# Kernel tuning notes

Hardware: AMD Instinct MI355X
Metric: run time of the kernel (lower is better)

Reference implementation:

```python
import jax, jax.numpy as jnp
import numpy as np

N_LEVELS = 8
BASE_RES = 16
LOG2_T = 14
T = 1 << LOG2_T
WIDTH, HEIGHT = 1024, 768
NUM_GAUSSIAN = 8
PRIME_Y = np.uint32(2654435761)
CORNERS = np.array([[0, 0], [1, 0], [0, 1], [1, 1]], dtype=np.uint32)


def _level_resolutions():
    bx = np.exp((np.log(WIDTH) - np.log(BASE_RES)) / (N_LEVELS - 1))
    by = np.exp((np.log(HEIGHT) - np.log(BASE_RES)) / (N_LEVELS - 1))
    return [(int(np.floor(BASE_RES * bx ** l)), int(np.floor(BASE_RES * by ** l)))
            for l in range(N_LEVELS)]


def hash_encode(x, hashidxs, table):
    # x: [N,2] in [0,1]; hashidxs: [N] int; table: [V, L, T, 2]
    feats = []
    offs = jnp.asarray(CORNERS)  # [4,2] uint32
    hv = hashidxs.astype(jnp.int32)[:, None]  # [N,1]
    for l, (rx, ry) in enumerate(_level_resolutions()):
        res = jnp.array([rx, ry], dtype=x.dtype)
        pos = x * res                      # [N,2]
        p0 = jnp.floor(pos)
        w = pos - p0                       # bilinear weights, [N,2]
        c = p0.astype(jnp.uint32)[:, None, :] + offs[None]  # [N,4,2]
        h = (c[..., 0] * jnp.uint32(1)) ^ (c[..., 1] * PRIME_Y)
        idx = (h & jnp.uint32(T - 1)).astype(jnp.int32)      # [N,4]
        f = table[hv, l, idx]              # [N,4,2] gather per corner
        wx, wy = w[:, 0:1], w[:, 1:2]
        ww = jnp.concatenate([(1 - wx) * (1 - wy), wx * (1 - wy),
                              (1 - wx) * wy, wx * wy], axis=1)  # [N,4]
        feats.append(jnp.sum(f * ww[..., None], axis=1))        # [N,2]
    return jnp.concatenate(feats, axis=-1)  # [N,16]


def gaussian_act(x, sigma=0.1):
    return jnp.exp(x * x * (-1.0 / (2.0 * sigma * sigma)))


def setup_inputs() -> dict:
    key = jax.random.key(0)
    ks = jax.random.split(key, 8)
    N = 2 ** 21
    V = 20
    x = jax.random.uniform(ks[0], (N, 2), dtype=jnp.float32)
    hashidxs = jax.random.randint(ks[1], (N,), 0, V, dtype=jnp.int32)
    color = jax.random.uniform(ks[2], (N, 3), dtype=jnp.float32)
    table = jax.random.normal(ks[3], (V, N_LEVELS, T, 2), dtype=jnp.float32) * 1e-2
    w1 = jax.random.normal(ks[4], (16, 32), dtype=jnp.float32) * (1.0 / np.sqrt(16))
    b1 = jax.random.normal(ks[5], (32,), dtype=jnp.float32) * 0.01
    w2 = jax.random.normal(ks[6], (32, 3 * NUM_GAUSSIAN), dtype=jnp.float32) * (1.0 / np.sqrt(32))
    b2 = jax.random.normal(ks[7], (3 * NUM_GAUSSIAN,), dtype=jnp.float32) * 0.01
    return {"x": x, "hashidxs": hashidxs, "color": color, "table": table,
            "w1": w1, "b1": b1, "w2": w2, "b2": b2}


def reference(x, hashidxs, color, table, w1, b1, w2, b2):
    H = hash_encode(x, hashidxs, table)            # [N,16]
    h1 = gaussian_act(H @ w1 + b1)                 # [N,32]
    raw = h1 @ w2 + b2                             # [N,24]
    G = NUM_GAUSSIAN
    weight = jnp.exp(raw[..., :G])
    mu = jax.nn.sigmoid(raw[..., G:2 * G])
    inv_sigma = jnp.exp(raw[..., 2 * G:3 * G])
    return mu, inv_sigma, weight, H
```

## Files before the change

### kernel.cpp

```cpp
#include <hip/hip_runtime.h>
#include <cmath>

#define NLEV 8
#define TSZ 16384
#define PRIME 2654435761u

struct Res { int rx[NLEV]; int ry[NLEV]; };

__global__ __launch_bounds__(256) void pg_kernel(
    const float* __restrict__ x,
    const int*   __restrict__ hashidxs,
    const float* __restrict__ table,
    const float* __restrict__ w1,
    const float* __restrict__ b1,
    const float* __restrict__ w2,
    const float* __restrict__ b2,
    float* __restrict__ out,
    int N, Res res)
{
    int i = blockIdx.x * blockDim.x + threadIdx.x;
    if (i >= N) return;

    float2 xv = ((const float2*)x)[i];
    int hv = hashidxs[i];
    const float* tb_base = table + (size_t)hv * (NLEV * TSZ * 2);

    float H[16];
    #pragma unroll
    for (int l = 0; l < NLEV; ++l) {
        float fx = (float)res.rx[l], fy = (float)res.ry[l];
        float posx = xv.x * fx, posy = xv.y * fy;
        float p0x = floorf(posx), p0y = floorf(posy);
        float wx = posx - p0x, wy = posy - p0y;
        unsigned cx = (unsigned)p0x, cy = (unsigned)p0y;
        const float* tb = tb_base + (size_t)l * (TSZ * 2);
        unsigned hy0 = cy * PRIME;
        unsigned hy1 = (cy + 1u) * PRIME;
        unsigned i00 = ( cx        ^ hy0) & (TSZ - 1);
        unsigned i10 = ((cx + 1u)  ^ hy0) & (TSZ - 1);
        unsigned i01 = ( cx        ^ hy1) & (TSZ - 1);
        unsigned i11 = ((cx + 1u)  ^ hy1) & (TSZ - 1);
        float2 f00 = *(const float2*)(tb + 2u * i00);
        float2 f10 = *(const float2*)(tb + 2u * i10);
        float2 f01 = *(const float2*)(tb + 2u * i01);
        float2 f11 = *(const float2*)(tb + 2u * i11);
        float w00 = (1.f - wx) * (1.f - wy);
        float w10 = wx * (1.f - wy);
        float w01 = (1.f - wx) * wy;
        float w11 = wx * wy;
        H[2*l]   = fmaf(f00.x, w00, fmaf(f10.x, w10, fmaf(f01.x, w01, f11.x * w11)));
        H[2*l+1] = fmaf(f00.y, w00, fmaf(f10.y, w10, fmaf(f01.y, w01, f11.y * w11)));
    }

    float h1[32];
    #pragma unroll
    for (int j = 0; j < 32; ++j) {
        float s = b1[j];
        #pragma unroll
        for (int k = 0; k < 16; ++k) s = fmaf(H[k], w1[k * 32 + j], s);
        h1[j] = __expf(-50.f * s * s);
    }

    float raw[24];
    #pragma unroll
    for (int j = 0; j < 24; ++j) {
        float s = b2[j];
        #pragma unroll
        for (int k = 0; k < 32; ++k) s = fmaf(h1[k], w2[k * 24 + j], s);
        raw[j] = s;
    }

    float wt[8], mu[8], isg[8];
    #pragma unroll
    for (int g = 0; g < 8; ++g) {
        wt[g]  = __expf(raw[g]);
        mu[g]  = 1.f / (1.f + __expf(-raw[8 + g]));
        isg[g] = __expf(raw[16 + g]);
    }

    size_t N8 = (size_t)N * 8;
    float4* o;
    o = (float4*)(out) + (size_t)i * 2;
    o[0] = make_float4(mu[0], mu[1], mu[2], mu[3]);
    o[1] = make_float4(mu[4], mu[5], mu[6], mu[7]);
    o = (float4*)(out + N8) + (size_t)i * 2;
    o[0] = make_float4(isg[0], isg[1], isg[2], isg[3]);
    o[1] = make_float4(isg[4], isg[5], isg[6], isg[7]);
    o = (float4*)(out + 2 * N8) + (size_t)i * 2;
    o[0] = make_float4(wt[0], wt[1], wt[2], wt[3]);
    o[1] = make_float4(wt[4], wt[5], wt[6], wt[7]);
    o = (float4*)(out + 3 * N8) + (size_t)i * 4;
    o[0] = make_float4(H[0],  H[1],  H[2],  H[3]);
    o[1] = make_float4(H[4],  H[5],  H[6],  H[7]);
    o[2] = make_float4(H[8],  H[9],  H[10], H[11]);
    o[3] = make_float4(H[12], H[13], H[14], H[15]);
}

extern "C" void kernel_launch(void* const* d_in, const int* in_sizes, int n_in,
                              void* d_out, int out_size, void* d_ws, size_t ws_size,
                              hipStream_t stream) {
    const float* x        = (const float*)d_in[0];
    const int*   hashidxs = (const int*)  d_in[1];
    const float* table    = (const float*)d_in[3];
    const float* w1       = (const float*)d_in[4];
    const float* b1       = (const float*)d_in[5];
    const float* w2       = (const float*)d_in[6];
    const float* b2       = (const float*)d_in[7];
    float* out = (float*)d_out;
    int N = in_sizes[0] / 2;

    Res res;
    double bx = std::exp((std::log((double)1024) - std::log((double)16)) / 7.0);
    double by = std::exp((std::log((double)768)  - std::log((double)16)) / 7.0);
    for (int l = 0; l < NLEV; ++l) {
        res.rx[l] = (int)std::floor(16.0 * std::pow(bx, (double)l));
        res.ry[l] = (int)std::floor(16.0 * std::pow(by, (double)l));
    }

    dim3 block(256), grid((unsigned)((N + 255) / 256));
    hipLaunchKernelGGL(pg_kernel, grid, block, 0, stream,
                       x, hashidxs, table, w1, b1, w2, b2, out, N, res);
}
```

Baseline: 675.8 us.

## Bucket points by hash table index and remap workgroups per XCD

Adds a counting-sort pre-pass (zero, histogram, scan, scatter) that groups points by their hash-table index. The main kernel then processes points in sorted order, so each workgroup touches mostly one 1 MB table slice. Workgroup IDs are also remapped so that consecutive sorted chunks land on the same XCD, keeping each XCD's L2 working set to a few tables. The cost is four extra launches, an extra pass over x and hashidxs, and output writes that become scattered rather than coalesced. If the workspace is too small it falls back to the original kernel.

```diff
diff --git a/kernel.cpp b/kernel.cpp
--- a/kernel.cpp
+++ b/kernel.cpp
@@ -4,25 +4,19 @@
 #define NLEV 8
 #define TSZ 16384
 #define PRIME 2654435761u
+#define NBINS 32
+
+typedef float fx2 __attribute__((ext_vector_type(2)));
 
 struct Res { int rx[NLEV]; int ry[NLEV]; };
 
-__global__ __launch_bounds__(256) void pg_kernel(
-    const float* __restrict__ x,
-    const int*   __restrict__ hashidxs,
+__device__ __forceinline__ void compute_point(
+    fx2 xv, int hv, int p,
     const float* __restrict__ table,
-    const float* __restrict__ w1,
-    const float* __restrict__ b1,
-    const float* __restrict__ w2,
-    const float* __restrict__ b2,
-    float* __restrict__ out,
-    int N, Res res)
-{
-    int i = blockIdx.x * blockDim.x + threadIdx.x;
-    if (i >= N) return;
-
-    float2 xv = ((const float2*)x)[i];
-    int hv = hashidxs[i];
+    const float* __restrict__ w1, const float* __restrict__ b1,
+    const float* __restrict__ w2, const float* __restrict__ b2,
+    float* __restrict__ out, int N, const Res& res)
+{
     const float* tb_base = table + (size_t)hv * (NLEV * TSZ * 2);
 
     float H[16];
@@ -40,10 +34,10 @@
         unsigned i10 = ((cx + 1u)  ^ hy0) & (TSZ - 1);
         unsigned i01 = ( cx        ^ hy1) & (TSZ - 1);
         unsigned i11 = ((cx + 1u)  ^ hy1) & (TSZ - 1);
-        float2 f00 = *(const float2*)(tb + 2u * i00);
-        float2 f10 = *(const float2*)(tb + 2u * i10);
-        float2 f01 = *(const float2*)(tb + 2u * i01);
-        float2 f11 = *(const float2*)(tb + 2u * i11);
+        fx2 f00 = *(const fx2*)(tb + 2u * i00);
+        fx2 f10 = *(const fx2*)(tb + 2u * i10);
+        fx2 f01 = *(const fx2*)(tb + 2u * i01);
+        fx2 f11 = *(const fx2*)(tb + 2u * i11);
         float w00 = (1.f - wx) * (1.f - wy);
         float w10 = wx * (1.f - wy);
         float w01 = (1.f - wx) * wy;
@@ -80,20 +74,102 @@
 
     size_t N8 = (size_t)N * 8;
     float4* o;
-    o = (float4*)(out) + (size_t)i * 2;
+    o = (float4*)(out) + (size_t)p * 2;
     o[0] = make_float4(mu[0], mu[1], mu[2], mu[3]);
     o[1] = make_float4(mu[4], mu[5], mu[6], mu[7]);
-    o = (float4*)(out + N8) + (size_t)i * 2;
+    o = (float4*)(out + N8) + (size_t)p * 2;
     o[0] = make_float4(isg[0], isg[1], isg[2], isg[3]);
     o[1] = make_float4(isg[4], isg[5], isg[6], isg[7]);
-    o = (float4*)(out + 2 * N8) + (size_t)i * 2;
+    o = (float4*)(out + 2 * N8) + (size_t)p * 2;
     o[0] = make_float4(wt[0], wt[1], wt[2], wt[3]);
     o[1] = make_float4(wt[4], wt[5], wt[6], wt[7]);
-    o = (float4*)(out + 3 * N8) + (size_t)i * 4;
+    o = (float4*)(out + 3 * N8) + (size_t)p * 4;
     o[0] = make_float4(H[0],  H[1],  H[2],  H[3]);
     o[1] = make_float4(H[4],  H[5],  H[6],  H[7]);
     o[2] = make_float4(H[8],  H[9],  H[10], H[11]);
     o[3] = make_float4(H[12], H[13], H[14], H[15]);
+}
+
+__global__ __launch_bounds__(256) void pg_kernel(
+    const float* __restrict__ x, const int* __restrict__ hashidxs,
+    const float* __restrict__ table,
+    const float* __restrict__ w1, const float* __restrict__ b1,
+    const float* __restrict__ w2, const float* __restrict__ b2,
+    float* __restrict__ out, int N, Res res)
+{
+    int i = blockIdx.x * blockDim.x + threadIdx.x;
+    if (i >= N) return;
+    fx2 xv = ((const fx2*)x)[i];
+    int hv = hashidxs[i];
+    compute_point(xv, hv, i, table, w1, b1, w2, b2, out, N, res);
+}
+
+__global__ void k_zero(int* __restrict__ c) {
+    int t = threadIdx.x;
+    if (t < 2 * NBINS) c[t] = 0;
+}
+
+__global__ __launch_bounds__(256) void k_hist(
+    const int* __restrict__ hashidxs, int N, int* __restrict__ hist)
+{
+    __shared__ int lh[NBINS];
+    int t = threadIdx.x;
+    if (t < NBINS) lh[t] = 0;
+    __syncthreads();
+    int i = blockIdx.x * 256 + t;
+    if (i < N) atomicAdd(&lh[hashidxs[i]], 1);
+    __syncthreads();
+    if (t < NBINS && lh[t]) atomicAdd(&hist[t], lh[t]);
+}
+
+__global__ void k_scan(const int* __restrict__ hist, int* __restrict__ cursor) {
+    if (threadIdx.x == 0 && blockIdx.x == 0) {
+        int acc = 0;
+        for (int b = 0; b < NBINS; ++b) { cursor[b] = acc; acc += hist[b]; }
+    }
+}
+
+__global__ __launch_bounds__(256) void k_scatter(
+    const float* __restrict__ x, const int* __restrict__ hashidxs, int N,
+    int* __restrict__ cursor, int* __restrict__ order, float* __restrict__ sx)
+{
+    __shared__ int lh[NBINS];
+    __shared__ int lbase[NBINS];
+    int t = threadIdx.x;
+    if (t < NBINS) lh[t] = 0;
+    __syncthreads();
+    int i = blockIdx.x * 256 + t;
+    int hv = -1, r = 0;
+    if (i < N) { hv = hashidxs[i]; r = atomicAdd(&lh[hv], 1); }
+    __syncthreads();
+    if (t < NBINS && lh[t]) lbase[t] = atomicAdd(&cursor[t], lh[t]);
+    __syncthreads();
+    if (i < N) {
+        int pos = lbase[hv] + r;
+        order[pos] = i | (hv << 24);
+        ((fx2*)sx)[pos] = ((const fx2*)x)[i];
+    }
+}
+
+__global__ __launch_bounds__(256) void pg_main(
+    const int*   __restrict__ order,
+    const float* __restrict__ sx,
+    const float* __restrict__ table,
+    const float* __restrict__ w1, const float* __restrict__ b1,
+    const float* __restrict__ w2, const float* __restrict__ b2,
+    float* __restrict__ out, int N, Res res)
+{
+    unsigned nwg  = gridDim.x, orig = blockIdx.x;
+    unsigned q = nwg / 8u, rr = nwg % 8u, xcd = orig % 8u;
+    unsigned wg = (xcd < rr ? xcd * (q + 1u) : rr * (q + 1u) + (xcd - rr) * q) + orig / 8u;
+    int j = (int)(wg * 256u + threadIdx.x);
+    if (j >= N) return;
+
+    int packed = order[j];
+    int p  = packed & 0xFFFFFF;
+    int hv = packed >> 24;
+    fx2 xv = ((const fx2*)sx)[j];
+    compute_point(xv, hv, p, table, w1, b1, w2, b2, out, N, res);
 }
 
 extern "C" void kernel_launch(void* const* d_in, const int* in_sizes, int n_in,
@@ -117,7 +193,29 @@
         res.ry[l] = (int)std::floor(16.0 * std::pow(by, (double)l));
     }
 
-    dim3 block(256), grid((unsigned)((N + 255) / 256));
-    hipLaunchKernelGGL(pg_kernel, grid, block, 0, stream,
-                       x, hashidxs, table, w1, b1, w2, b2, out, N, res);
-}
+    dim3 block(256);
+    unsigned nwg = (unsigned)((N + 255) / 256);
+    dim3 grid(nwg);
+
+    size_t order_off = 1024;
+    size_t sx_off    = order_off + (((size_t)N * 4 + 255) & ~(size_t)255);
+    size_t ws_need   = sx_off + (size_t)N * 8;
+
+    if (ws_size < ws_need || N >= (1 << 24)) {
+        hipLaunchKernelGGL(pg_kernel, grid, block, 0, stream,
+                           x, hashidxs, table, w1, b1, w2, b2, out, N, res);
+        return;
+    }
+
+    int*   hist   = (int*)d_ws;
+    int*   cursor = (int*)d_ws + NBINS;
+    int*   order  = (int*)((char*)d_ws + order_off);
+    float* sx     = (float*)((char*)d_ws + sx_off);
+
+    hipLaunchKernelGGL(k_zero,    dim3(1),   dim3(64),  0, stream, hist);
+    hipLaunchKernelGGL(k_hist,    grid,      block,     0, stream, hashidxs, N, hist);
+    hipLaunchKernelGGL(k_scan,    dim3(1),   dim3(32),  0, stream, hist, cursor);
+    hipLaunchKernelGGL(k_scatter, grid,      block,     0, stream, x, hashidxs, N, cursor, order, sx);
+    hipLaunchKernelGGL(pg_main,   grid,      block,     0, stream,
+                       order, sx, table, w1, b1, w2, b2, out, N, res);
+}
```

Result: slower. 832.3 us (+23.2%).
